# Kernel optimization log

Measured on AMD Instinct MI355X. Metric: run time of the kernel, lower is better.

Reference implementation:

```python
import jax, jax.numpy as jnp
import numpy as np

ALPHA = 4.0  # spikingjelly default Sigmoid surrogate alpha
BN_EPS = 1e-5

@jax.custom_vjp
def spike(x):
    return (x >= 0.0).astype(x.dtype)

def _spike_fwd(x):
    return spike(x), x

def _spike_bwd(res, g):
    s = jax.nn.sigmoid(ALPHA * res)
    return (g * ALPHA * s * (1.0 - s),)

spike.defvjp(_spike_fwd, _spike_bwd)

def lif(x, tau=2.0, vth=1.0):
    # MultiStepLIFNode: hard reset (v_reset=0), detach_reset=True, scan over time axis 0
    def step(v, xt):
        h = v + (xt - v) / tau          # charge
        s = spike(h - vth)              # fire (surrogate grad)
        v_next = h * (1.0 - jax.lax.stop_gradient(s))  # detached hard reset to 0
        return v_next, s
    _, out = jax.lax.scan(step, jnp.zeros_like(x[0]), x)
    return out

def conv_bn(x, w, b, g, be, m, var):
    # x: [TB, C, N]; 1x1 Conv1d is a channel GEMM, then eval-mode BatchNorm1d
    y = jnp.einsum('oc,bcn->bon', w, x) + b[None, :, None]
    inv = g / jnp.sqrt(var + BN_EPS)
    return (y - m[None, :, None]) * inv[None, :, None] + be[None, :, None]

def setup_inputs() -> dict:
    key = jax.random.key(0)
    T, B, C, H, W = 4, 32, 512, 14, 14
    ks = jax.random.split(key, 32)
    d = {'x': jax.random.normal(ks[0], (T, B, C, H, W), dtype=jnp.float32)}
    scale = 1.0 / np.sqrt(C)
    i = 1
    for p in ['q', 'k', 'v', 'p']:
        d[p + '_cw'] = jax.random.normal(ks[i], (C, C), dtype=jnp.float32) * scale; i += 1
        d[p + '_cb'] = jax.random.normal(ks[i], (C,), dtype=jnp.float32) * 0.1; i += 1
        d[p + '_bg'] = jnp.ones((C,), dtype=jnp.float32)
        d[p + '_bb'] = jnp.zeros((C,), dtype=jnp.float32)
        d[p + '_bm'] = jax.random.normal(ks[i], (C,), dtype=jnp.float32) * 0.1; i += 1
        d[p + '_bv'] = jax.random.uniform(ks[i], (C,), dtype=jnp.float32, minval=0.5, maxval=1.5); i += 1
    d['push_w'] = jnp.asarray(1.0, dtype=jnp.float32)
    d['pull_w'] = jnp.asarray(1.0, dtype=jnp.float32)
    d['pp_bias'] = jnp.asarray(0.0, dtype=jnp.float32)
    return d

def reference(x,
              q_cw, q_cb, q_bg, q_bb, q_bm, q_bv,
              k_cw, k_cb, k_bg, k_bb, k_bm, k_bv,
              v_cw, v_cb, v_bg, v_bb, v_bm, v_bv,
              p_cw, p_cb, p_bg, p_bb, p_bm, p_bv,
              push_w, pull_w, pp_bias):
    T, B, C, H, W = x.shape
    N = H * W
    nh = 8
    hd = C // nh
    scale = 0.125

    xs = lif(x)                                   # head_lif, [T,B,C,H,W]
    xf = xs.reshape(T * B, C, N)
    q = conv_bn(xf, q_cw, q_cb, q_bg, q_bb, q_bm, q_bv).reshape(T, B, C, N)
    k = conv_bn(xf, k_cw, k_cb, k_bg, k_bb, k_bm, k_bv).reshape(T, B, C, N)
    v = conv_bn(xf, v_cw, v_cb, v_bg, v_bb, v_bm, v_bv).reshape(T, B, C, N)

    q_on = lif(q)
    q_off = lif(-q)

    def to_heads(t):  # [T,B,C,N] -> [T,B,nh,N,hd]
        return jnp.swapaxes(t, -1, -2).reshape(T, B, N, nh, hd).transpose(0, 1, 3, 2, 4)

    q_on_h = to_heads(q_on)
    q_off_h = to_heads(q_off)
    k_h = to_heads(lif(k))
    v_h = to_heads(lif(v))

    pw = jax.nn.softplus(push_w)
    pl = jax.nn.softplus(pull_w)
    diff = pw * q_on_h - pl * q_off_h + pp_bias   # push-pull gating
    q_pp = lif(diff)

    kv = jnp.einsum('tbhnd,tbhne->tbhde', k_h, v_h)      # k^T @ v, [T,B,h,hd,hd]
    o = jnp.einsum('tbhnd,tbhde->tbhne', q_pp, kv) * scale

    o = o.transpose(0, 1, 2, 4, 3).reshape(T, B, C, N)   # transpose(3,4) then merge heads
    o = lif(o, vth=0.5)                                   # attn_lif
    o = conv_bn(o.reshape(T * B, C, N), p_cw, p_cb, p_bg, p_bb, p_bm, p_bv)
    return o.reshape(T, B, C, H, W)
```

## Files before the change

### kernel.cpp

```cpp
#include <hip/hip_runtime.h>
#include <hip/hip_bf16.h>
#include <math.h>

typedef unsigned short u16;
typedef unsigned int   u32;

#define CC 512
#define NN 196
#define TT 4
#define BB 32
#define TBB 128
#define NHH 8
#define HD 64

#define ROWS_T  6272
#define CSTRIDE ((size_t)ROWS_T * CC)

typedef __attribute__((ext_vector_type(8))) _Float16 f16x8;
typedef __attribute__((ext_vector_type(4))) float f32x4;

#define ONE_H 0x3C00

__device__ __forceinline__ u16 h_bits(_Float16 h) { return *(u16*)&h; }
__device__ __forceinline__ float h2f(u16 u) { return (float)(*(const _Float16*)&u); }
__device__ __forceinline__ u32 pk2(u16 a, u16 b) { return (u32)a | ((u32)b << 16); }

__device__ __forceinline__ void gld16(const void* g, void* l) {
    __builtin_amdgcn_global_load_lds(
        (const __attribute__((address_space(1))) void*)g,
        (__attribute__((address_space(3))) void*)l, 16, 0, 0);
}

__global__ __launch_bounds__(256) void k_prep(
    const float* __restrict__ qw, const float* __restrict__ kw,
    const float* __restrict__ vw, const float* __restrict__ pw,
    const float* __restrict__ cb0, const float* __restrict__ bg0, const float* __restrict__ bb0,
    const float* __restrict__ bm0, const float* __restrict__ bv0,
    const float* __restrict__ cb1, const float* __restrict__ bg1, const float* __restrict__ bb1,
    const float* __restrict__ bm1, const float* __restrict__ bv1,
    const float* __restrict__ cb2, const float* __restrict__ bg2, const float* __restrict__ bb2,
    const float* __restrict__ bm2, const float* __restrict__ bv2,
    const float* __restrict__ cb3, const float* __restrict__ bg3, const float* __restrict__ bb3,
    const float* __restrict__ bm3, const float* __restrict__ bv3,
    u16* __restrict__ W2, float* __restrict__ SS, float* __restrict__ SH) {
    if (blockIdx.x < 4096) {
        size_t idx = (size_t)blockIdx.x * 256 + threadIdx.x;
        int g = (int)(idx >> 18);
        size_t rem = idx & 262143;
        const float* Ws = (g == 0) ? qw : (g == 1) ? kw : (g == 2) ? vw : pw;
        float w  = Ws[rem];
        _Float16 h0 = (fabsf(w) < 6.2e-5f) ? (_Float16)0.0f : (_Float16)w;
        float r = (w - (float)h0) * 2048.0f;
        _Float16 h1 = (_Float16)r;
        size_t base = (size_t)g * 524288 + rem;
        W2[base] = h_bits(h0); W2[base + 262144] = h_bits(h1);
        return;
    }
    int idx = (blockIdx.x - 4096) * 256 + threadIdx.x;
    int g = idx >> 9, o = idx & 511;
    const float* cb = g == 0 ? cb0 : g == 1 ? cb1 : g == 2 ? cb2 : cb3;
    const float* bg = g == 0 ? bg0 : g == 1 ? bg1 : g == 2 ? bg2 : bg3;
    const float* bb = g == 0 ? bb0 : g == 1 ? bb1 : g == 2 ? bb2 : bb3;
    const float* bm = g == 0 ? bm0 : g == 1 ? bm1 : g == 2 ? bm2 : bm3;
    const float* bv = g == 0 ? bv0 : g == 1 ? bv1 : g == 2 ? bv2 : bv3;
    float inv = bg[o] / sqrtf(bv[o] + 1e-5f);
    SS[g * 512 + o] = inv;
    SH[g * 512 + o] = (cb[o] - bm[o]) * inv + bb[o];
}

__global__ __launch_bounds__(256) void k_head_lif(const float* __restrict__ x, u16* __restrict__ XS) {
    __shared__ float T[64][65];
    const int tid = threadIdx.x;
    const int n0 = blockIdx.x * 64;
    const int b  = blockIdx.y;
    const int c_base = blockIdx.z * 64;
    const int c_l = tid >> 4;
    const int n4  = (tid & 15) * 4;
    const bool lv = (n0 + n4) < NN;
    const int n_r = tid >> 2;
    const int cq  = (tid & 3) * 16;
    const bool wv = (n0 + n_r) < NN;

    float v[4][4];
    #pragma unroll
    for (int k = 0; k < 4; ++k)
        #pragma unroll
        for (int j = 0; j < 4; ++j) v[k][j] = 0.f;

    for (int t = 0; t < TT; ++t) {
        const size_t xb = ((size_t)(t * BB + b) * CC + c_base) * NN;
        float s[4][4];
        #pragma unroll
        for (int k = 0; k < 4; ++k) {
            const int c = c_l + 16 * k;
            float4 xv = make_float4(0.f, 0.f, 0.f, 0.f);
            if (lv) xv = *(const float4*)(x + xb + (size_t)c * NN + n0 + n4);
            float xa[4] = {xv.x, xv.y, xv.z, xv.w};
            #pragma unroll
            for (int j = 0; j < 4; ++j) {
                float h = v[k][j] + (xa[j] - v[k][j]) * 0.5f;
                s[k][j] = (h >= 1.f) ? 1.f : 0.f;
                v[k][j] = (h >= 1.f) ? 0.f : h;
            }
        }
        __syncthreads();
        #pragma unroll
        for (int k = 0; k < 4; ++k)
            #pragma unroll
            for (int j = 0; j < 4; ++j) T[c_l + 16 * k][n4 + j] = s[k][j];
        __syncthreads();
        if (wv) {
            const size_t ob = ((size_t)(t * BB + b) * NN + n0 + n_r) * CC + c_base + cq;
            u16 u[16];
            #pragma unroll
            for (int m = 0; m < 16; ++m) u[m] = (T[cq + m][n_r] != 0.f) ? ONE_H : 0;
            uint4 q0 = make_uint4(pk2(u[0],u[1]),  pk2(u[2],u[3]),  pk2(u[4],u[5]),  pk2(u[6],u[7]));
            uint4 q1 = make_uint4(pk2(u[8],u[9]),  pk2(u[10],u[11]),pk2(u[12],u[13]),pk2(u[14],u[15]));
            *(uint4*)(XS + ob)     = q0;
            *(uint4*)(XS + ob + 8) = q1;
        }
        __syncthreads();
    }
}

#define YSTRIDE_F 13631488
__global__ __launch_bounds__(256) void k_gemm_qkv(const u16* __restrict__ S, const u16* __restrict__ W2,
                                                  const float* __restrict__ scale, const float* __restrict__ shift,
                                                  float* __restrict__ Y) {
    __shared__ __align__(16) u16 Xt[128 * 64];
    __shared__ __align__(16) u16 Wt[2][128 * 64];
    const int tid  = threadIdx.x;
    const int lane = tid & 63;
    const int w    = tid >> 6;
    const int bid  = blockIdx.x;
    const int work = (bid & 7) * 294 + (bid >> 3);
    const int ntile = work / 12;
    const int gw    = work - ntile * 12;
    const int g     = gw >> 2;
    const int wtile = gw & 3;
    const u16* Sb = S + (size_t)ntile * 128 * CC;
    const u16* Wb = W2 + (size_t)g * 524288 + (size_t)(wtile * 128) * CC;
    const float* scl = scale + g * 512;
    const float* shf = shift + g * 512;
    float* Yg = Y + (size_t)g * YSTRIDE_F;

    const int lrow8  = lane >> 3;
    const int gchunk = ((lane & 7) ^ lrow8) * 8;
    const int l15 = lane & 15;
    const int q4  = lane >> 4;
    const int wm = (w >> 1) * 64, wn = (w & 1) * 64;

    f32x4 acc[4][4];
    f32x4 zz = {0.f, 0.f, 0.f, 0.f};
    #pragma unroll
    for (int i = 0; i < 4; ++i)
        #pragma unroll
        for (int j = 0; j < 4; ++j) acc[i][j] = zz;

    for (int c0 = 0; c0 < CC; c0 += 64) {
        __syncthreads();
        #pragma unroll
        for (int i = 0; i < 4; ++i) {
            int p = w * 4 + i;
            gld16(Sb + (size_t)(p * 8 + lrow8) * CC + c0 + gchunk, &Xt[p * 512]);
        }
        #pragma unroll
        for (int i = 0; i < 8; ++i) {
            int lin = w * 8 + i;
            int s = lin >> 4, p = lin & 15;
            gld16(Wb + (size_t)s * 262144 + (size_t)(p * 8 + lrow8) * CC + c0 + gchunk,
                  &Wt[s][p * 512]);
        }
        __syncthreads();

        #pragma unroll
        for (int ks = 0; ks < 2; ++ks) {
            const int cpo = ((ks * 4 + q4) ^ (l15 & 7)) * 8;
            f16x8 sf[4], sflo[4];
            #pragma unroll
            for (int i = 0; i < 4; ++i) {
                sf[i]   = *(const f16x8*)&Xt[(wm + i * 16 + l15) * 64 + cpo];
                sflo[i] = sf[i] * (_Float16)0.00048828125f;
            }
            #pragma unroll
            for (int s = 0; s < 2; ++s) {
                f16x8 wf[4];
                #pragma unroll
                for (int i = 0; i < 4; ++i)
                    wf[i] = *(const f16x8*)&Wt[s][(wn + i * 16 + l15) * 64 + cpo];
                #pragma unroll
                for (int mt = 0; mt < 4; ++mt)
                    #pragma unroll
                    for (int nt = 0; nt < 4; ++nt)
                        acc[mt][nt] = __builtin_amdgcn_mfma_f32_16x16x32_f16(
                            s ? sflo[mt] : sf[mt], wf[nt], acc[mt][nt], 0, 0, 0);
            }
        }
    }

    #pragma unroll
    for (int nt = 0; nt < 4; ++nt) {
        int o = wtile * 128 + wn + nt * 16 + l15;
        float sc = scl[o], sh = shf[o];
        #pragma unroll
        for (int mt = 0; mt < 4; ++mt) {
            int r0 = ntile * 128 + wm + mt * 16 + (lane >> 4) * 4;
            #pragma unroll
            for (int r = 0; r < 4; ++r)
                Yg[(size_t)(r0 + r) * CC + o] = acc[mt][nt][r] * sc + sh;
        }
    }
}

__global__ __launch_bounds__(256) void k_lif_all(const float4* __restrict__ Yq, const float4* __restrict__ Yk,
                                                 const float4* __restrict__ Yv, uint4* __restrict__ QS,
                                                 uint4* __restrict__ KS, uint4* __restrict__ VS,
                                                 const float* __restrict__ pw_,
                                                 const float* __restrict__ pl_,
                                                 const float* __restrict__ pb_) {
    const size_t idx = (size_t)blockIdx.x * 256 + threadIdx.x;
    const float pw = log1pf(expf(pw_[0]));
    const float pl = log1pf(expf(pl_[0]));
    const float pb = pb_[0];
    float von[8], voff[8], vpp[8], vk[8], vv[8];
    #pragma unroll
    for (int j = 0; j < 8; ++j) { von[j] = voff[j] = vpp[j] = vk[j] = vv[j] = 0.f; }
    #pragma unroll
    for (int t = 0; t < TT; ++t) {
        const size_t o4 = idx * 2 + (size_t)t * (CSTRIDE / 4);
        float4 q0 = Yq[o4], q1 = Yq[o4 + 1];
        float4 k0 = Yk[o4], k1 = Yk[o4 + 1];
        float4 x0 = Yv[o4], x1 = Yv[o4 + 1];
        float qa[8] = {q0.x, q0.y, q0.z, q0.w, q1.x, q1.y, q1.z, q1.w};
        float ka[8] = {k0.x, k0.y, k0.z, k0.w, k1.x, k1.y, k1.z, k1.w};
        float xa[8] = {x0.x, x0.y, x0.z, x0.w, x1.x, x1.y, x1.z, x1.w};
        u16 uq[8], uk[8], uv[8];
        #pragma unroll
        for (int j = 0; j < 8; ++j) {
            float h;
            h = von[j]  + ( qa[j] - von[j] ) * 0.5f; bool s1 = (h >= 1.f); von[j]  = s1 ? 0.f : h;
            h = voff[j] + (-qa[j] - voff[j]) * 0.5f; bool s2 = (h >= 1.f); voff[j] = s2 ? 0.f : h;
            float diff = pw * (s1 ? 1.f : 0.f) - pl * (s2 ? 1.f : 0.f) + pb;
            h = vpp[j]  + (diff - vpp[j]) * 0.5f; bool sp = (h >= 1.f); vpp[j]  = sp ? 0.f : h;
            h = vk[j]   + (ka[j] - vk[j] ) * 0.5f; bool sk = (h >= 1.f); vk[j]   = sk ? 0.f : h;
            h = vv[j]   + (xa[j] - vv[j] ) * 0.5f; bool sv = (h >= 1.f); vv[j]   = sv ? 0.f : h;
            uq[j] = sp ? ONE_H : 0; uk[j] = sk ? ONE_H : 0; uv[j] = sv ? ONE_H : 0;
        }
        const size_t o8 = idx + (size_t)t * (CSTRIDE / 8);
        QS[o8] = make_uint4(pk2(uq[0],uq[1]), pk2(uq[2],uq[3]), pk2(uq[4],uq[5]), pk2(uq[6],uq[7]));
        KS[o8] = make_uint4(pk2(uk[0],uk[1]), pk2(uk[2],uk[3]), pk2(uk[4],uk[5]), pk2(uk[6],uk[7]));
        VS[o8] = make_uint4(pk2(uv[0],uv[1]), pk2(uv[2],uv[3]), pk2(uv[4],uv[5]), pk2(uv[6],uv[7]));
    }
}

__global__ __launch_bounds__(256) void k_attn(const u16* __restrict__ Q, const u16* __restrict__ K,
                                              const u16* __restrict__ V, u16* __restrict__ OS) {
    __shared__ __align__(16) u16 sm[19584];
    u16* Kt  = sm;
    u16* Vt  = sm + 8704;
    u16* Qs  = sm;
    u16* kvT = sm + 14976;

    const int tid = threadIdx.x;
    const int tb  = blockIdx.x >> 3;
    const int h   = blockIdx.x & 7;
    const size_t gb = (size_t)tb * NN * CC + (size_t)h * HD;

    const int srow = tid >> 2;
    const int sdq  = (tid & 3) * 16;

    const int lane = tid & 63;
    const int w    = tid >> 6;
    const int l15  = lane & 15;
    const int kb8  = (lane >> 4) * 8;
    const int quad = (lane >> 4) * 4;
    const int dh = (w >> 1) * 32, eh = (w & 1) * 32;

    f32x4 accA[2][2];
    f32x4 zz = {0.f, 0.f, 0.f, 0.f};
    #pragma unroll
    for (int i = 0; i < 2; ++i)
        #pragma unroll
        for (int j = 0; j < 2; ++j) accA[i][j] = zz;

    const uint4 z4 = make_uint4(0, 0, 0, 0);

    #pragma unroll
    for (int ch = 0; ch < 2; ++ch) {
        if (ch) __syncthreads();
        #pragma unroll
        for (int c = 0; c < 2; ++c) {
            int n  = ch * 128 + c * 64 + srow;
            int nl = c * 64 + srow;
            bool valid = n < NN;
            const u16* kr = K + gb + (size_t)n * CC + sdq;
            const u16* vr = V + gb + (size_t)n * CC + sdq;
            uint4 ka  = valid ? *(const uint4*)kr : z4;
            uint4 kb2 = valid ? *(const uint4*)(kr + 8) : z4;
            uint4 va  = valid ? *(const uint4*)vr : z4;
            uint4 vb2 = valid ? *(const uint4*)(vr + 8) : z4;
            u32 kwv[8] = {ka.x, ka.y, ka.z, ka.w, kb2.x, kb2.y, kb2.z, kb2.w};
            u32 vwv[8] = {va.x, va.y, va.z, va.w, vb2.x, vb2.y, vb2.z, vb2.w};
            #pragma unroll
            for (int i = 0; i < 8; ++i) {
                Kt[(sdq + 2 * i) * 136 + nl]     = (u16)(kwv[i] & 0xFFFF);
                Kt[(sdq + 2 * i + 1) * 136 + nl] = (u16)(kwv[i] >> 16);
                Vt[(sdq + 2 * i) * 136 + nl]     = (u16)(vwv[i] & 0xFFFF);
                Vt[(sdq + 2 * i + 1) * 136 + nl] = (u16)(vwv[i] >> 16);
            }
        }
        __syncthreads();
        #pragma unroll
        for (int k0 = 0; k0 < 128; k0 += 32) {
            f16x8 af[2], bv[2];
            #pragma unroll
            for (int i = 0; i < 2; ++i) {
                af[i] = *(const f16x8*)&Kt[(dh + i * 16 + l15) * 136 + k0 + kb8];
                bv[i] = *(const f16x8*)&Vt[(eh + i * 16 + l15) * 136 + k0 + kb8];
            }
            #pragma unroll
            for (int i = 0; i < 2; ++i)
                #pragma unroll
                for (int j = 0; j < 2; ++j)
                    accA[i][j] = __builtin_amdgcn_mfma_f32_16x16x32_f16(af[i], bv[j], accA[i][j], 0, 0, 0);
        }
    }
    __syncthreads();

    #pragma unroll
    for (int i = 0; i < 2; ++i)
        #pragma unroll
        for (int j = 0; j < 2; ++j)
            #pragma unroll
            for (int r = 0; r < 4; ++r) {
                int e = eh + j * 16 + l15;
                int d = dh + i * 16 + quad + r;
                _Float16 hv = (_Float16)accA[i][j][r];
                kvT[e * 72 + d] = h_bits(hv);
            }
    #pragma unroll
    for (int p = 0; p < 4; ++p) {
        int n = p * 64 + srow;
        if (n < 208) {
            if (n < NN) {
                const u16* qr = Q + gb + (size_t)n * CC + sdq;
                uint4 qa  = *(const uint4*)qr;
                uint4 qb2 = *(const uint4*)(qr + 8);
                u32 qwv[8] = {qa.x, qa.y, qa.z, qa.w, qb2.x, qb2.y, qb2.z, qb2.w};
                #pragma unroll
                for (int i = 0; i < 8; ++i) {
                    Qs[n * 72 + sdq + 2 * i]     = (u16)(qwv[i] & 0xFFFF);
                    Qs[n * 72 + sdq + 2 * i + 1] = (u16)(qwv[i] >> 16);
                }
            } else {
                #pragma unroll
                for (int i = 0; i < 16; ++i) Qs[n * 72 + sdq + i] = 0;
            }
        }
    }
    __syncthreads();

    f16x8 bq0 = *(const f16x8*)&kvT[(w * 16 + l15) * 72 + 0  + kb8];
    f16x8 bq1 = *(const f16x8*)&kvT[(w * 16 + l15) * 72 + 32 + kb8];
    u16* ob = OS + (size_t)tb * NN * CC + (size_t)h * HD + w * 16 + l15;
    #pragma unroll
    for (int nt = 0; nt < 13; ++nt) {
        f32x4 acc = zz;
        f16x8 a0 = *(const f16x8*)&Qs[(nt * 16 + l15) * 72 + 0  + kb8];
        f16x8 a1 = *(const f16x8*)&Qs[(nt * 16 + l15) * 72 + 32 + kb8];
        acc = __builtin_amdgcn_mfma_f32_16x16x32_f16(a0, bq0, acc, 0, 0, 0);
        acc = __builtin_amdgcn_mfma_f32_16x16x32_f16(a1, bq1, acc, 0, 0, 0);
        #pragma unroll
        for (int r = 0; r < 4; ++r) {
            int n = nt * 16 + quad + r;
            if (n < NN) {
                _Float16 ov = (_Float16)(acc[r] * 0.125f);
                ob[(size_t)n * CC] = h_bits(ov);
            }
        }
    }
}

__global__ __launch_bounds__(256) void k_attn_lif(uint4* __restrict__ OS) {
    const size_t idx = (size_t)blockIdx.x * 256 + threadIdx.x;
    float v[8];
    #pragma unroll
    for (int j = 0; j < 8; ++j) v[j] = 0.f;
    #pragma unroll
    for (int t = 0; t < TT; ++t) {
        const size_t o8 = idx + (size_t)t * (CSTRIDE / 8);
        uint4 d = OS[o8];
        u32 dw[4] = {d.x, d.y, d.z, d.w};
        u16 u[8];
        #pragma unroll
        for (int p = 0; p < 4; ++p) {
            #pragma unroll
            for (int hf = 0; hf < 2; ++hf) {
                int j = p * 2 + hf;
                u16 raw = hf ? (u16)(dw[p] >> 16) : (u16)(dw[p] & 0xFFFF);
                float xv = h2f(raw);
                float h = v[j] + (xv - v[j]) * 0.5f;
                bool s = (h >= 0.5f);
                v[j] = s ? 0.f : h;
                u[j] = s ? ONE_H : 0;
            }
        }
        OS[o8] = make_uint4(pk2(u[0],u[1]), pk2(u[2],u[3]), pk2(u[4],u[5]), pk2(u[6],u[7]));
    }
}

__global__ __launch_bounds__(256) void k_gemm_proj(const u16* __restrict__ S, const u16* __restrict__ W2,
                                                   const float* __restrict__ scale, const float* __restrict__ shift,
                                                   float* __restrict__ Y) {
    __shared__ __align__(16) u16 Xt[128 * 64];
    __shared__ __align__(16) u16 Wt[2][128 * 64];
    const int tid  = threadIdx.x;
    const int lane = tid & 63;
    const int w    = tid >> 6;
    const int bid  = blockIdx.x;
    const int work = (bid & 7) * 98 + (bid >> 3);
    const int ntile = work >> 2;
    const int wtile = work & 3;
    const u16* Sb = S + (size_t)ntile * 128 * CC;
    const u16* Wb = W2 + (size_t)(wtile * 128) * CC;

    const int lrow8  = lane >> 3;
    const int gchunk = ((lane & 7) ^ lrow8) * 8;
    const int l15 = lane & 15;
    const int q4  = lane >> 4;
    const int wm = (w >> 1) * 64, wn = (w & 1) * 64;

    const int tb0 = (ntile * 128) / NN;
    const int bnd = (tb0 + 1) * NN;

    f32x4 acc[4][4];
    f32x4 zz = {0.f, 0.f, 0.f, 0.f};
    #pragma unroll
    for (int i = 0; i < 4; ++i)
        #pragma unroll
        for (int j = 0; j < 4; ++j) acc[i][j] = zz;

    for (int c0 = 0; c0 < CC; c0 += 64) {
        __syncthreads();
        #pragma unroll
        for (int i = 0; i < 4; ++i) {
            int p = w * 4 + i;
            gld16(Sb + (size_t)(p * 8 + lrow8) * CC + c0 + gchunk, &Xt[p * 512]);
        }
        #pragma unroll
        for (int i = 0; i < 8; ++i) {
            int lin = w * 8 + i;
            int s = lin >> 4, p = lin & 15;
            gld16(Wb + (size_t)s * 262144 + (size_t)(p * 8 + lrow8) * CC + c0 + gchunk,
                  &Wt[s][p * 512]);
        }
        __syncthreads();

        #pragma unroll
        for (int ks = 0; ks < 2; ++ks) {
            const int cpo = ((ks * 4 + q4) ^ (l15 & 7)) * 8;
            f16x8 sf[4], sflo[4];
            #pragma unroll
            for (int i = 0; i < 4; ++i) {
                sf[i]   = *(const f16x8*)&Xt[(wn + i * 16 + l15) * 64 + cpo];
                sflo[i] = sf[i] * (_Float16)0.00048828125f;
            }
            #pragma unroll
            for (int s = 0; s < 2; ++s) {
                f16x8 wf[4];
                #pragma unroll
                for (int i = 0; i < 4; ++i)
                    wf[i] = *(const f16x8*)&Wt[s][(wm + i * 16 + l15) * 64 + cpo];
                #pragma unroll
                for (int mt = 0; mt < 4; ++mt)
                    #pragma unroll
                    for (int nt = 0; nt < 4; ++nt)
                        acc[mt][nt] = __builtin_amdgcn_mfma_f32_16x16x32_f16(
                            wf[mt], s ? sflo[nt] : sf[nt], acc[mt][nt], 0, 0, 0);
            }
        }
    }

    #pragma unroll
    for (int mt = 0; mt < 4; ++mt) {
        int o0 = wtile * 128 + wm + mt * 16 + (lane >> 4) * 4;
        #pragma unroll
        for (int nt = 0; nt < 4; ++nt) {
            int row = ntile * 128 + wn + nt * 16 + l15;
            int tb = (row >= bnd) ? tb0 + 1 : tb0;
            int n  = row - tb * NN;
            #pragma unroll
            for (int r = 0; r < 4; ++r)
                Y[((size_t)tb * CC + o0 + r) * NN + n] = acc[mt][nt][r] * scale[o0 + r] + shift[o0 + r];
        }
    }
}

extern "C" void kernel_launch(void* const* d_in, const int* in_sizes, int n_in,
                              void* d_out, int out_size, void* d_ws, size_t ws_size,
                              hipStream_t stream) {
    const float* x    = (const float*)d_in[0];
    const float* q_cw = (const float*)d_in[1];
    const float* q_cb = (const float*)d_in[2];
    const float* q_bg = (const float*)d_in[3];
    const float* q_bb = (const float*)d_in[4];
    const float* q_bm = (const float*)d_in[5];
    const float* q_bv = (const float*)d_in[6];
    const float* k_cw = (const float*)d_in[7];
    const float* k_cb = (const float*)d_in[8];
    const float* k_bg = (const float*)d_in[9];
    const float* k_bb = (const float*)d_in[10];
    const float* k_bm = (const float*)d_in[11];
    const float* k_bv = (const float*)d_in[12];
    const float* v_cw = (const float*)d_in[13];
    const float* v_cb = (const float*)d_in[14];
    const float* v_bg = (const float*)d_in[15];
    const float* v_bb = (const float*)d_in[16];
    const float* v_bm = (const float*)d_in[17];
    const float* v_bv = (const float*)d_in[18];
    const float* p_cw = (const float*)d_in[19];
    const float* p_cb = (const float*)d_in[20];
    const float* p_bg = (const float*)d_in[21];
    const float* p_bb = (const float*)d_in[22];
    const float* p_bm = (const float*)d_in[23];
    const float* p_bv = (const float*)d_in[24];
    const float* pshw = (const float*)d_in[25];
    const float* pllw = (const float*)d_in[26];
    const float* ppb  = (const float*)d_in[27];
    float* out = (float*)d_out;

    if (ws_size < (size_t)242 * 1024 * 1024) return;
    char* W = (char*)d_ws;
    u16*   XS = (u16*)W;
    u16*   QS = (u16*)W;
    float* Yq = (float*)(W + ((size_t)26 << 20));
    float* Yk = (float*)(W + ((size_t)78 << 20));
    float* Yv = (float*)(W + ((size_t)130 << 20));
    u16*   KS = (u16*)(W + ((size_t)182 << 20));
    u16*   VS = (u16*)(W + ((size_t)208 << 20));
    u16*   OS = (u16*)(W + ((size_t)26 << 20));
    u16*   W2 = (u16*)(W + ((size_t)234 << 20));
    float* SS = (float*)(W + ((size_t)238 << 20));
    float* SH = SS + 2048;

    k_prep<<<4104, 256, 0, stream>>>(q_cw, k_cw, v_cw, p_cw,
                                     q_cb, q_bg, q_bb, q_bm, q_bv,
                                     k_cb, k_bg, k_bb, k_bm, k_bv,
                                     v_cb, v_bg, v_bb, v_bm, v_bv,
                                     p_cb, p_bg, p_bb, p_bm, p_bv, W2, SS, SH);

    k_head_lif<<<dim3(4, 32, 8), 256, 0, stream>>>(x, XS);

    k_gemm_qkv<<<2352, 256, 0, stream>>>(XS, W2, SS, SH, Yq);

    k_lif_all<<<1568, 256, 0, stream>>>((const float4*)Yq, (const float4*)Yk, (const float4*)Yv,
                                        (uint4*)QS, (uint4*)KS, (uint4*)VS, pshw, pllw, ppb);

    k_attn<<<TBB * NHH, 256, 0, stream>>>(QS, KS, VS, OS);
    k_attn_lif<<<1568, 256, 0, stream>>>((uint4*)OS);

    k_gemm_proj<<<784, 256, 0, stream>>>(OS, W2 + 3 * 524288, SS + 1536, SH + 1536, out);
}
```

Measured before the change: 354.4 us.

## Fuse LIF spiking into QKV GEMM epilogue with time-grouped row tiles

Retiles the QKV GEMM so each block's 128 M-rows hold 32 spatial positions across all 4 timesteps of one batch. This lets the epilogue run the LIF and push-pull scans over time directly from shared memory. It removes the float32 Yq/Yk/Yv intermediates (about 150 MB of writes and reads) and the separate k_lif_all kernel. In exchange, the last N tile is padded (196 of 224 rows used), so the grid and GEMM work grow, and the epilogue writes narrow 4-byte strided stores.

```diff
diff --git a/kernel.cpp b/kernel.cpp
--- a/kernel.cpp
+++ b/kernel.cpp
@@ -123,26 +123,29 @@
     }
 }
 
-#define YSTRIDE_F 13631488
 __global__ __launch_bounds__(256) void k_gemm_qkv(const u16* __restrict__ S, const u16* __restrict__ W2,
                                                   const float* __restrict__ scale, const float* __restrict__ shift,
-                                                  float* __restrict__ Y) {
-    __shared__ __align__(16) u16 Xt[128 * 64];
-    __shared__ __align__(16) u16 Wt[2][128 * 64];
+                                                  u16* __restrict__ QS, u16* __restrict__ KS, u16* __restrict__ VS,
+                                                  const float* __restrict__ PW, const float* __restrict__ PL,
+                                                  const float* __restrict__ PB) {
+    __shared__ __align__(16) u16 smem[24576];
+    u16* Xt  = smem;
+    u16* WtF = smem + 8192;
     const int tid  = threadIdx.x;
     const int lane = tid & 63;
     const int w    = tid >> 6;
     const int bid  = blockIdx.x;
-    const int work = (bid & 7) * 294 + (bid >> 3);
-    const int ntile = work / 12;
-    const int gw    = work - ntile * 12;
-    const int g     = gw >> 2;
+    const int work = (bid & 7) * 336 + (bid >> 3);
+    const int b    = work / 84;
+    const int rem  = work - b * 84;
+    const int nt7  = rem / 12;
+    const int gw   = rem - nt7 * 12;
+    const int g    = gw >> 2;
     const int wtile = gw & 3;
-    const u16* Sb = S + (size_t)ntile * 128 * CC;
+    const int n0   = nt7 * 32;
     const u16* Wb = W2 + (size_t)g * 524288 + (size_t)(wtile * 128) * CC;
     const float* scl = scale + g * 512;
     const float* shf = shift + g * 512;
-    float* Yg = Y + (size_t)g * YSTRIDE_F;
 
     const int lrow8  = lane >> 3;
     const int gchunk = ((lane & 7) ^ lrow8) * 8;
@@ -150,6 +153,8 @@
     const int q4  = lane >> 4;
     const int wm = (w >> 1) * 64, wn = (w & 1) * 64;
 
+    const size_t arow0 = ((size_t)(w * 32 + b) * NN + n0) * CC;
+
     f32x4 acc[4][4];
     f32x4 zz = {0.f, 0.f, 0.f, 0.f};
     #pragma unroll
@@ -162,14 +167,14 @@
         #pragma unroll
         for (int i = 0; i < 4; ++i) {
             int p = w * 4 + i;
-            gld16(Sb + (size_t)(p * 8 + lrow8) * CC + c0 + gchunk, &Xt[p * 512]);
+            gld16(S + arow0 + (size_t)(i * 8 + lrow8) * CC + c0 + gchunk, &Xt[p * 512]);
         }
         #pragma unroll
         for (int i = 0; i < 8; ++i) {
             int lin = w * 8 + i;
             int s = lin >> 4, p = lin & 15;
             gld16(Wb + (size_t)s * 262144 + (size_t)(p * 8 + lrow8) * CC + c0 + gchunk,
-                  &Wt[s][p * 512]);
+                  WtF + s * 8192 + p * 512);
         }
         __syncthreads();
 
@@ -187,7 +192,7 @@
                 f16x8 wf[4];
                 #pragma unroll
                 for (int i = 0; i < 4; ++i)
-                    wf[i] = *(const f16x8*)&Wt[s][(wn + i * 16 + l15) * 64 + cpo];
+                    wf[i] = *(const f16x8*)&WtF[s * 8192 + (wn + i * 16 + l15) * 64 + cpo];
                 #pragma unroll
                 for (int mt = 0; mt < 4; ++mt)
                     #pragma unroll
@@ -198,58 +203,81 @@
         }
     }
 
-    #pragma unroll
-    for (int nt = 0; nt < 4; ++nt) {
-        int o = wtile * 128 + wn + nt * 16 + l15;
-        float sc = scl[o], sh = shf[o];
-        #pragma unroll
-        for (int mt = 0; mt < 4; ++mt) {
-            int r0 = ntile * 128 + wm + mt * 16 + (lane >> 4) * 4;
-            #pragma unroll
-            for (int r = 0; r < 4; ++r)
-                Yg[(size_t)(r0 + r) * CC + o] = acc[mt][nt][r] * sc + sh;
-        }
-    }
-}
-
-__global__ __launch_bounds__(256) void k_lif_all(const float4* __restrict__ Yq, const float4* __restrict__ Yk,
-                                                 const float4* __restrict__ Yv, uint4* __restrict__ QS,
-                                                 uint4* __restrict__ KS, uint4* __restrict__ VS,
-                                                 const float* __restrict__ pw_,
-                                                 const float* __restrict__ pl_,
-                                                 const float* __restrict__ pb_) {
-    const size_t idx = (size_t)blockIdx.x * 256 + threadIdx.x;
-    const float pw = log1pf(expf(pw_[0]));
-    const float pl = log1pf(expf(pl_[0]));
-    const float pb = pb_[0];
-    float von[8], voff[8], vpp[8], vk[8], vv[8];
-    #pragma unroll
-    for (int j = 0; j < 8; ++j) { von[j] = voff[j] = vpp[j] = vk[j] = vv[j] = 0.f; }
-    #pragma unroll
-    for (int t = 0; t < TT; ++t) {
-        const size_t o4 = idx * 2 + (size_t)t * (CSTRIDE / 4);
-        float4 q0 = Yq[o4], q1 = Yq[o4 + 1];
-        float4 k0 = Yk[o4], k1 = Yk[o4 + 1];
-        float4 x0 = Yv[o4], x1 = Yv[o4 + 1];
-        float qa[8] = {q0.x, q0.y, q0.z, q0.w, q1.x, q1.y, q1.z, q1.w};
-        float ka[8] = {k0.x, k0.y, k0.z, k0.w, k1.x, k1.y, k1.z, k1.w};
-        float xa[8] = {x0.x, x0.y, x0.z, x0.w, x1.x, x1.y, x1.z, x1.w};
-        u16 uq[8], uk[8], uv[8];
-        #pragma unroll
-        for (int j = 0; j < 8; ++j) {
-            float h;
-            h = von[j]  + ( qa[j] - von[j] ) * 0.5f; bool s1 = (h >= 1.f); von[j]  = s1 ? 0.f : h;
-            h = voff[j] + (-qa[j] - voff[j]) * 0.5f; bool s2 = (h >= 1.f); voff[j] = s2 ? 0.f : h;
-            float diff = pw * (s1 ? 1.f : 0.f) - pl * (s2 ? 1.f : 0.f) + pb;
-            h = vpp[j]  + (diff - vpp[j]) * 0.5f; bool sp = (h >= 1.f); vpp[j]  = sp ? 0.f : h;
-            h = vk[j]   + (ka[j] - vk[j] ) * 0.5f; bool sk = (h >= 1.f); vk[j]   = sk ? 0.f : h;
-            h = vv[j]   + (xa[j] - vv[j] ) * 0.5f; bool sv = (h >= 1.f); vv[j]   = sv ? 0.f : h;
-            uq[j] = sp ? ONE_H : 0; uk[j] = sk ? ONE_H : 0; uv[j] = sv ? ONE_H : 0;
-        }
-        const size_t o8 = idx + (size_t)t * (CSTRIDE / 8);
-        QS[o8] = make_uint4(pk2(uq[0],uq[1]), pk2(uq[2],uq[3]), pk2(uq[4],uq[5]), pk2(uq[6],uq[7]));
-        KS[o8] = make_uint4(pk2(uk[0],uk[1]), pk2(uk[2],uk[3]), pk2(uk[4],uk[5]), pk2(uk[6],uk[7]));
-        VS[o8] = make_uint4(pk2(uv[0],uv[1]), pk2(uv[2],uv[3]), pk2(uv[4],uv[5]), pk2(uv[6],uv[7]));
+    const float pwv = (g == 0) ? log1pf(expf(PW[0])) : 0.f;
+    const float plv = (g == 0) ? log1pf(expf(PL[0])) : 0.f;
+    const float pbv = (g == 0) ? PB[0] : 0.f;
+    u16* OUT = (g == 0) ? QS : (g == 1) ? KS : VS;
+    float* LY = (float*)smem;
+    const int pairid = w & 1;
+    const int pr  = tid >> 7;
+    const int idx = tid & 127;
+
+    #pragma unroll
+    for (int cc = 0; cc < 2; ++cc) {
+        __syncthreads();
+        #pragma unroll
+        for (int ntl = 0; ntl < 2; ++ntl) {
+            const int nt = cc * 2 + ntl;
+            const int o  = wtile * 128 + wn + nt * 16 + l15;
+            const float sc = scl[o], sh = shf[o];
+            const int col32 = ntl * 16 + l15;
+            #pragma unroll
+            for (int mt = 0; mt < 4; ++mt) {
+                const int tr0 = wm + mt * 16 + q4 * 4;
+                #pragma unroll
+                for (int r = 0; r < 4; ++r)
+                    LY[(pairid * 128 + tr0 + r) * 33 + col32] = acc[mt][nt][r] * sc + sh;
+            }
+        }
+        __syncthreads();
+        #pragma unroll
+        for (int stp = 0; stp < 4; ++stp) {
+            const int chain = stp * 128 + idx;
+            const int nn  = chain >> 4;
+            const int c2  = (chain & 15) * 2;
+            const int n   = n0 + nn;
+            const float* Lp = &LY[(pr * 128 + nn) * 33 + c2];
+            float ya[4][2];
+            #pragma unroll
+            for (int t = 0; t < 4; ++t) {
+                ya[t][0] = Lp[t * 32 * 33];
+                ya[t][1] = Lp[t * 32 * 33 + 1];
+            }
+            if (n < NN) {
+                const int ocol = wtile * 128 + pr * 64 + cc * 32 + c2;
+                u32* op = (u32*)(OUT + (size_t)(b * NN + n) * CC + ocol);
+                if (g == 0) {
+                    float von[2] = {0.f, 0.f}, voff[2] = {0.f, 0.f}, vpp[2] = {0.f, 0.f};
+                    #pragma unroll
+                    for (int t = 0; t < 4; ++t) {
+                        u16 sp2[2];
+                        #pragma unroll
+                        for (int j = 0; j < 2; ++j) {
+                            float qv = ya[t][j], h;
+                            h = von[j]  + ( qv - von[j] ) * 0.5f; bool s1 = (h >= 1.f); von[j]  = s1 ? 0.f : h;
+                            h = voff[j] + (-qv - voff[j]) * 0.5f; bool s2 = (h >= 1.f); voff[j] = s2 ? 0.f : h;
+                            float diff = pwv * (s1 ? 1.f : 0.f) - plv * (s2 ? 1.f : 0.f) + pbv;
+                            h = vpp[j] + (diff - vpp[j]) * 0.5f; bool sp = (h >= 1.f); vpp[j] = sp ? 0.f : h;
+                            sp2[j] = sp ? ONE_H : 0;
+                        }
+                        op[t * (CSTRIDE / 2)] = pk2(sp2[0], sp2[1]);
+                    }
+                } else {
+                    float vm[2] = {0.f, 0.f};
+                    #pragma unroll
+                    for (int t = 0; t < 4; ++t) {
+                        u16 s2[2];
+                        #pragma unroll
+                        for (int j = 0; j < 2; ++j) {
+                            float h = vm[j] + (ya[t][j] - vm[j]) * 0.5f;
+                            bool s = (h >= 1.f); vm[j] = s ? 0.f : h;
+                            s2[j] = s ? ONE_H : 0;
+                        }
+                        op[t * (CSTRIDE / 2)] = pk2(s2[0], s2[1]);
+                    }
+                }
+            }
+        }
     }
 }
 
@@ -532,13 +560,10 @@
     if (ws_size < (size_t)242 * 1024 * 1024) return;
     char* W = (char*)d_ws;
     u16*   XS = (u16*)W;
-    u16*   QS = (u16*)W;
-    float* Yq = (float*)(W + ((size_t)26 << 20));
-    float* Yk = (float*)(W + ((size_t)78 << 20));
-    float* Yv = (float*)(W + ((size_t)130 << 20));
+    u16*   QS = (u16*)(W + ((size_t)27 << 20));
+    u16*   OS = (u16*)(W + ((size_t)78 << 20));
     u16*   KS = (u16*)(W + ((size_t)182 << 20));
     u16*   VS = (u16*)(W + ((size_t)208 << 20));
-    u16*   OS = (u16*)(W + ((size_t)26 << 20));
     u16*   W2 = (u16*)(W + ((size_t)234 << 20));
     float* SS = (float*)(W + ((size_t)238 << 20));
     float* SH = SS + 2048;
@@ -551,10 +576,7 @@
 
     k_head_lif<<<dim3(4, 32, 8), 256, 0, stream>>>(x, XS);
 
-    k_gemm_qkv<<<2352, 256, 0, stream>>>(XS, W2, SS, SH, Yq);
-
-    k_lif_all<<<1568, 256, 0, stream>>>((const float4*)Yq, (const float4*)Yk, (const float4*)Yv,
-                                        (uint4*)QS, (uint4*)KS, (uint4*)VS, pshw, pllw, ppb);
+    k_gemm_qkv<<<2688, 256, 0, stream>>>(XS, W2, SS, SH, QS, KS, VS, pshw, pllw, ppb);
 
     k_attn<<<TBB * NHH, 256, 0, stream>>>(QS, KS, VS, OS);
     k_attn_lif<<<1568, 256, 0, stream>>>((uint4*)OS);
```

After: 332.5 us. 6.2% less time.
